# Performance work log

Measured on AMD Instinct MI355X. Metric: run time of the kernel, lower is better.

The kernel has to match this reference:

```python
import jax, jax.numpy as jnp
import numpy as np

NUM_EXPERTS = 8
TOP_K = 2
N_TOKENS = 4096
HIDDEN = 1024
EXPERT_DIM = 4096


def setup_inputs() -> dict:
    key = jax.random.key(0)
    ks = jax.random.split(key, 4)
    x = jax.random.normal(ks[0], (N_TOKENS, HIDDEN), dtype=jnp.float32)
    Wg = jax.random.normal(ks[1], (HIDDEN, NUM_EXPERTS), dtype=jnp.float32) * 0.02
    bg = jnp.zeros((NUM_EXPERTS,), dtype=jnp.float32)
    W1 = jax.random.normal(ks[2], (NUM_EXPERTS, HIDDEN, EXPERT_DIM), dtype=jnp.float32) * 0.02
    b1 = jnp.zeros((NUM_EXPERTS, EXPERT_DIM), dtype=jnp.float32)
    W2 = jax.random.normal(ks[3], (NUM_EXPERTS, EXPERT_DIM, HIDDEN), dtype=jnp.float32) * 0.02
    b2 = jnp.zeros((NUM_EXPERTS, HIDDEN), dtype=jnp.float32)
    return {"x": x, "Wg": Wg, "bg": bg, "W1": W1, "b1": b1, "W2": W2, "b2": b2}


def reference(x, Wg, bg, W1, b1, W2, b2):
    # Gating: softmax over experts, then top-k routing with renormalized gates.
    gate_probs = jax.nn.softmax(x @ Wg + bg, axis=-1)          # [N, E]
    top_gates, top_idx = jax.lax.top_k(gate_probs, TOP_K)      # [N, K]
    top_gates = top_gates / jnp.sum(top_gates, axis=-1, keepdims=True)
    # Per-(token, expert) combine weight: sum of gates routed to that expert.
    combine = jnp.sum(
        jax.nn.one_hot(top_idx, NUM_EXPERTS, dtype=x.dtype) * top_gates[..., None],
        axis=1,
    )  # [N, E]
    # Expert MLPs: Linear -> ReLU -> Linear (dropout=0 at eval, norm=False).
    out = jnp.zeros_like(x)
    for e in range(NUM_EXPERTS):
        h = jax.nn.relu(x @ W1[e] + b1[e])                      # [N, expert_dim]
        y = h @ W2[e] + b2[e]                                   # [N, hidden]
        out = out + combine[:, e:e + 1] * y
    # Switch-style auxiliary load-balancing loss.
    expert_counts = jnp.sum(gate_probs, axis=0)                 # [E]
    expert_fractions = expert_counts / jnp.sum(expert_counts)
    gate_means = jnp.mean(gate_probs, axis=0)
    aux_loss = NUM_EXPERTS * jnp.sum(expert_fractions * gate_means)
    return out, aux_loss
```

## Files before the change

kernel.cpp:

```cpp
#include <hip/hip_runtime.h>


typedef unsigned short u16;
typedef __bf16 bf16x8 __attribute__((ext_vector_type(8)));
typedef float  f32x4  __attribute__((ext_vector_type(4)));

#define NTOK 4096
#define HID  1024
#define EDIM 4096
#define NEXP 8
#define MAXMT 72

__device__ __forceinline__ u16 f32_bf16(float f) {
  unsigned int u = __float_as_uint(f);
  u += 0x7FFFu + ((u >> 16) & 1u);
  return (u16)(u >> 16);
}

__global__ void gate_kernel(const float* __restrict__ x,
                            const float* __restrict__ Wg,
                            const float* __restrict__ bg,
                            float* __restrict__ combine,
                            float* __restrict__ counts,
                            int* __restrict__ icnt,
                            int* __restrict__ top2idx,
                            float* __restrict__ top2g,
                            u16* __restrict__ xbf) {
  __shared__ float lc[NEXP];
  int t = threadIdx.x;
  if (t < NEXP) lc[t] = 0.f;
  __syncthreads();
  int token = blockIdx.x * 4 + (t >> 6);
  int lane = t & 63;
  float s[NEXP] = {};
  const float* xr = x + (size_t)token * HID;
  u16* xb = xbf + (size_t)token * HID;
  for (int h = lane; h < HID; h += 64) {
    float xv = xr[h];
    xb[h] = f32_bf16(xv);
    const float* wrow = Wg + (size_t)h * NEXP;
#pragma unroll
    for (int e = 0; e < NEXP; ++e) s[e] += xv * wrow[e];
  }
#pragma unroll
  for (int off = 32; off > 0; off >>= 1) {
#pragma unroll
    for (int e = 0; e < NEXP; ++e) s[e] += __shfl_xor(s[e], off);
  }
  float m = -1e30f;
#pragma unroll
  for (int e = 0; e < NEXP; ++e) { s[e] += bg[e]; m = fmaxf(m, s[e]); }
  float p[NEXP]; float sum = 0.f;
#pragma unroll
  for (int e = 0; e < NEXP; ++e) { p[e] = expf(s[e] - m); sum += p[e]; }
  float inv = 1.f / sum;
#pragma unroll
  for (int e = 0; e < NEXP; ++e) p[e] *= inv;
  int i1 = 0; float g1 = p[0];
#pragma unroll
  for (int e = 1; e < NEXP; ++e) if (p[e] > g1) { g1 = p[e]; i1 = e; }
  int i2 = -1; float g2 = -1.f;
#pragma unroll
  for (int e = 0; e < NEXP; ++e) if (e != i1 && p[e] > g2) { g2 = p[e]; i2 = e; }
  float ginv = 1.f / (g1 + g2);
  if (lane == 0) {
#pragma unroll
    for (int e = 0; e < NEXP; ++e) {
      float c = (e == i1) ? g1 * ginv : (e == i2) ? g2 * ginv : 0.f;
      combine[(size_t)token * NEXP + e] = c;
      atomicAdd(&lc[e], p[e]);
    }
    top2idx[token * 2] = i1; top2idx[token * 2 + 1] = i2;
    top2g[token * 2] = g1 * ginv; top2g[token * 2 + 1] = g2 * ginv;
    atomicAdd(&icnt[i1], 1); atomicAdd(&icnt[i2], 1);
  }
  __syncthreads();
  if (t < NEXP) atomicAdd(&counts[t], lc[t]);
}

__global__ void aux_kernel(const float* __restrict__ counts, float* __restrict__ aux_out) {
  float s = 0.f;
#pragma unroll
  for (int e = 0; e < NEXP; ++e) s += counts[e];
  float a = 0.f;
#pragma unroll
  for (int e = 0; e < NEXP; ++e) a += (counts[e] / s) * (counts[e] / (float)NTOK);
  aux_out[0] = (float)NEXP * a;
}

__global__ void route_kernel(const int* __restrict__ icnt,
                             const float* __restrict__ counts,
                             const int* __restrict__ top2idx,
                             int* __restrict__ nmtP,
                             int* __restrict__ mtE, int* __restrict__ mtRow0,
                             int* __restrict__ mtValid,
                             int* __restrict__ tok,
                             float* __restrict__ aux_out) {
  __shared__ int l_off[NEXP];
  __shared__ int l_cur[NEXP];
  int t = threadIdx.x;
  if (t == 0) {
    int s = 0, nm = 0;
    for (int e = 0; e < NEXP; ++e) {
      l_off[e] = s; l_cur[e] = 0;
      int c = icnt[e];
      int tiles = (c + 127) >> 7;
      for (int mt = 0; mt < tiles; ++mt) {
        mtE[nm] = e; mtRow0[nm] = s + (mt << 7);
        int v = c - (mt << 7); mtValid[nm] = v > 128 ? 128 : v;
        nm++;
      }
      s += c;
    }
    nmtP[0] = nm;
    float fs = 0.f;
    for (int e = 0; e < NEXP; ++e) fs += counts[e];
    float a = 0.f;
    for (int e = 0; e < NEXP; ++e) a += (counts[e] / fs) * (counts[e] / (float)NTOK);
    aux_out[0] = (float)NEXP * a;
  }
  __syncthreads();
  for (int i = t; i < NTOK * 2; i += 256) {
    int e = top2idx[i];
    int pos = atomicAdd(&l_cur[e], 1);
    tok[l_off[e] + pos] = (i >> 1) | ((i & 1) << 16);
  }
}

__global__ __launch_bounds__(256) void cvtT_kernel(const float* __restrict__ W,
                                                   u16* __restrict__ WT, int R, int C) {
  __shared__ u16 tile[64][66];
  int t = threadIdx.x;
  size_t eoff = (size_t)blockIdx.z * R * C;
  int c0 = blockIdx.x * 64, r0 = blockIdx.y * 64;
  const float* Wp = W + eoff + (size_t)r0 * C + c0;
  u16* WTp = WT + eoff + (size_t)c0 * R + r0;
#pragma unroll
  for (int p = 0; p < 4; ++p) {
    int idx = p * 256 + t;
    int row = idx >> 4;
    int col = (idx & 15) * 4;
    float4 v = *(const float4*)(Wp + (size_t)row * C + col);
    tile[row][col + 0] = f32_bf16(v.x);
    tile[row][col + 1] = f32_bf16(v.y);
    tile[row][col + 2] = f32_bf16(v.z);
    tile[row][col + 3] = f32_bf16(v.w);
  }
  __syncthreads();
#pragma unroll
  for (int p = 0; p < 4; ++p) {
    int idx = p * 256 + t;
    int oc = idx >> 4;
    int orow = (idx & 15) * 4;
    ushort4 o;
    o.x = tile[orow + 0][oc];
    o.y = tile[orow + 1][oc];
    o.z = tile[orow + 2][oc];
    o.w = tile[orow + 3][oc];
    *(ushort4*)(WTp + (size_t)oc * R + orow) = o;
  }
}

template<int MODE, int SPLITK>
__global__ __launch_bounds__(256) void gemm_sparse(
    const u16* __restrict__ A, const u16* __restrict__ Wt,
    const int* __restrict__ nmtP, const int* __restrict__ mtE,
    const int* __restrict__ mtRow0, const int* __restrict__ mtValid,
    const int* __restrict__ tok,
    const float* __restrict__ bias, u16* __restrict__ Hout,
    float* __restrict__ Y0, float* __restrict__ Y1)
{
  constexpr int KDIM = (MODE == 1) ? HID : EDIM;
  constexpr int NDIM = (MODE == 1) ? EDIM : HID;
  constexpr int NT = NDIM / 128;
  constexpr int NK = KDIM / 32 / SPLITK;

  const int nwg = gridDim.x;
  const int q = nwg >> 3, rr8 = nwg & 7;
  const int xcd = blockIdx.x & 7, jj = blockIdx.x >> 3;
  int item = (xcd < rr8 ? xcd * (q + 1) : rr8 * (q + 1) + (xcd - rr8) * q) + jj;

  if (item >= nmtP[0] * NT * SPLITK) return;
  const int gmt = item / (NT * SPLITK);
  const int sk  = (item / NT) % SPLITK;
  const int nt  = item % NT;
  const int e = mtE[gmt], row0 = mtRow0[gmt], valid = mtValid[gmt];
  const int kbeg = sk * (KDIM / SPLITK);

  __shared__ __align__(16) u16 As[3][128 * 32];
  __shared__ __align__(16) u16 Bs[3][128 * 32];
  const int t = threadIdx.x;
  const int lane = t & 63;
  const int w = t >> 6;
  const int wr = w >> 1, wc = w & 1;
  const int bn0 = nt << 7;
  const int kq = lane >> 4;
  const int r  = lane & 15;

  const u16* Bb = Wt + ((size_t)e * NDIM + bn0) * KDIM;

  size_t arow[2];
  int srow[2];
#pragma unroll
  for (int c = 0; c < 2; ++c) {
    int idx = c * 256 + t;
    int row = idx >> 2;
    srow[c] = row;
    if (MODE == 1) {
      int rw = (row < valid) ? row : 0;
      arow[c] = (size_t)(tok[row0 + rw] & 0xFFFF) * KDIM;
    } else {
      arow[c] = (size_t)(row0 + row) * KDIM;
    }
  }

  auto stage = [&](int buf, int k0) {
#pragma unroll
    for (int c = 0; c < 2; ++c) {
      int idx = c * 256 + t;
      int row = idx >> 2;
      int kc  = (((idx & 3) ^ ((row >> 1) & 3))) << 3;
      __builtin_amdgcn_global_load_lds(
          (const __attribute__((address_space(1))) void*)(A + arow[c] + k0 + kc),
          (__attribute__((address_space(3))) void*)(&As[buf][idx * 8]), 16, 0, 0);
      __builtin_amdgcn_global_load_lds(
          (const __attribute__((address_space(1))) void*)(Bb + (size_t)srow[c] * KDIM + k0 + kc),
          (__attribute__((address_space(3))) void*)(&Bs[buf][idx * 8]), 16, 0, 0);
    }
  };

  f32x4 acc[4][4] = {};

  stage(0, kbeg);
  stage(1, kbeg + 32);
  int cb = 0, sb = 2;
  for (int ks = 0; ks < NK; ++ks) {
    if (ks + 1 < NK) asm volatile("s_waitcnt vmcnt(4)" ::: "memory");
    else             asm volatile("s_waitcnt vmcnt(0)" ::: "memory");
    __builtin_amdgcn_s_barrier();
    __builtin_amdgcn_sched_barrier(0);
    if (ks + 2 < NK) stage(sb, kbeg + (ks + 2) * 32);

    bf16x8 af[4], bfr[4];
#pragma unroll
    for (int f = 0; f < 4; ++f) {
      int ra = wr * 64 + f * 16 + r;
      af[f]  = *(const bf16x8*)(&As[cb][ra * 32 + ((kq ^ ((ra >> 1) & 3)) << 3)]);
      int rb = wc * 64 + f * 16 + r;
      bfr[f] = *(const bf16x8*)(&Bs[cb][rb * 32 + ((kq ^ ((rb >> 1) & 3)) << 3)]);
    }
    __builtin_amdgcn_s_setprio(1);
#pragma unroll
    for (int fm = 0; fm < 4; ++fm) {
#pragma unroll
      for (int fn = 0; fn < 4; ++fn) {
        acc[fn][fm] = __builtin_amdgcn_mfma_f32_16x16x32_bf16(bfr[fn], af[fm], acc[fn][fm], 0, 0, 0);
      }
    }
    __builtin_amdgcn_s_setprio(0);
    cb = (cb == 2) ? 0 : cb + 1;
    sb = (sb == 2) ? 0 : sb + 1;
  }

  if (MODE == 1) {
#pragma unroll
    for (int fm = 0; fm < 4; ++fm) {
      int lr = wr * 64 + fm * 16 + r;
      if (lr < valid) {
        u16* hrow = Hout + (size_t)(row0 + lr) * EDIM;
#pragma unroll
        for (int fn = 0; fn < 4; ++fn) {
          int col0 = bn0 + wc * 64 + fn * 16 + kq * 4;
          float4 bv = *(const float4*)(bias + (size_t)e * EDIM + col0);
          float v0 = acc[fn][fm][0] + bv.x; v0 = v0 > 0.f ? v0 : 0.f;
          float v1 = acc[fn][fm][1] + bv.y; v1 = v1 > 0.f ? v1 : 0.f;
          float v2 = acc[fn][fm][2] + bv.z; v2 = v2 > 0.f ? v2 : 0.f;
          float v3 = acc[fn][fm][3] + bv.w; v3 = v3 > 0.f ? v3 : 0.f;
          ushort4 h = make_ushort4(f32_bf16(v0), f32_bf16(v1), f32_bf16(v2), f32_bf16(v3));
          *(ushort4*)(hrow + col0) = h;
        }
      }
    }
  } else {
    float* Yb = (sk == 0) ? Y0 : Y1;
#pragma unroll
    for (int fm = 0; fm < 4; ++fm) {
      int lr = wr * 64 + fm * 16 + r;
      if (lr < valid) {
        int entry = tok[row0 + lr];
        int tt = entry & 0xFFFF, ss = entry >> 16;
        float* yrow = Yb + ((size_t)ss * NTOK + tt) * HID;
#pragma unroll
        for (int fn = 0; fn < 4; ++fn) {
          int col0 = bn0 + wc * 64 + fn * 16 + kq * 4;
          float4 o;
          if (sk == 0) {
            float4 bv = *(const float4*)(bias + (size_t)e * HID + col0);
            o.x = acc[fn][fm][0] + bv.x;
            o.y = acc[fn][fm][1] + bv.y;
            o.z = acc[fn][fm][2] + bv.z;
            o.w = acc[fn][fm][3] + bv.w;
          } else {
            o.x = acc[fn][fm][0];
            o.y = acc[fn][fm][1];
            o.z = acc[fn][fm][2];
            o.w = acc[fn][fm][3];
          }
          *(float4*)(yrow + col0) = o;
        }
      }
    }
  }
}

__global__ void final_kernel(const float* __restrict__ top2g,
                             const float* __restrict__ Ys0,
                             const float* __restrict__ Ys1,
                             float* __restrict__ out) {
  size_t idx4 = (size_t)blockIdx.x * 256 + threadIdx.x;
  size_t base = idx4 * 4;
  int t = (int)(base >> 10);
  float g0 = top2g[t * 2], g1 = top2g[t * 2 + 1];
  float4 a0 = *(const float4*)(Ys0 + base);
  float4 b0 = *(const float4*)(Ys1 + base);
  float4 a1 = *(const float4*)(Ys0 + (size_t)NTOK * HID + base);
  float4 b1 = *(const float4*)(Ys1 + (size_t)NTOK * HID + base);
  float4 o;
  o.x = g0 * (a0.x + b0.x) + g1 * (a1.x + b1.x);
  o.y = g0 * (a0.y + b0.y) + g1 * (a1.y + b1.y);
  o.z = g0 * (a0.z + b0.z) + g1 * (a1.z + b1.z);
  o.w = g0 * (a0.w + b0.w) + g1 * (a1.w + b1.w);
  *(float4*)(out + base) = o;
}

__global__ void init_out_kernel(const float* __restrict__ combine,
                                const float* __restrict__ b2,
                                float* __restrict__ out) {
  size_t idx = (size_t)blockIdx.x * 256 + threadIdx.x;
  int i = (int)(idx >> 10), j = (int)(idx & 1023);
  float v = 0.f;
#pragma unroll
  for (int e = 0; e < NEXP; ++e) v += combine[(size_t)i * NEXP + e] * b2[e * HID + j];
  out[idx] = v;
}

template<int MODE>
__global__ __launch_bounds__(256) void gemm_kernel(
    const u16* __restrict__ A, const u16* __restrict__ BT,
    int M, int N, int K,
    const float* __restrict__ bias, u16* __restrict__ Hout,
    const float* __restrict__ combine, int expert, float* __restrict__ Out)
{
  __shared__ __align__(16) u16 As[128 * 32];
  __shared__ __align__(16) u16 Bs[128 * 32];
  const int t = threadIdx.x;
  const int lane = t & 63;
  const int w = t >> 6;
  const int wr = w >> 1, wc = w & 1;
  const int nbn = N >> 7;
  const int bm0 = (int)(blockIdx.x / nbn) << 7;
  const int bn0 = (int)(blockIdx.x % nbn) << 7;
  const int kq = lane >> 4;
  const int r  = lane & 15;
  f32x4 acc[4][4] = {};
  const u16* Ab = A + (size_t)bm0 * K;
  const u16* Bb = BT + (size_t)bn0 * K;
  for (int k0 = 0; k0 < K; k0 += 32) {
    __syncthreads();
#pragma unroll
    for (int c = 0; c < 2; ++c) {
      int idx = c * 256 + t;
      int row = idx >> 2;
      int kc  = (idx & 3) << 3;
      __builtin_amdgcn_global_load_lds(
          (const __attribute__((address_space(1))) void*)(Ab + (size_t)row * K + k0 + kc),
          (__attribute__((address_space(3))) void*)(As + idx * 8), 16, 0, 0);
      __builtin_amdgcn_global_load_lds(
          (const __attribute__((address_space(1))) void*)(Bb + (size_t)row * K + k0 + kc),
          (__attribute__((address_space(3))) void*)(Bs + idx * 8), 16, 0, 0);
    }
    __syncthreads();
    bf16x8 af[4], bfr[4];
#pragma unroll
    for (int f = 0; f < 4; ++f) {
      af[f]  = *(const bf16x8*)(As + (wr * 64 + f * 16 + r) * 32 + kq * 8);
      bfr[f] = *(const bf16x8*)(Bs + (wc * 64 + f * 16 + r) * 32 + kq * 8);
    }
#pragma unroll
    for (int fm = 0; fm < 4; ++fm) {
#pragma unroll
      for (int fn = 0; fn < 4; ++fn) {
        acc[fm][fn] = __builtin_amdgcn_mfma_f32_16x16x32_bf16(af[fm], bfr[fn], acc[fm][fn], 0, 0, 0);
      }
    }
  }
  if (MODE == 1) {
#pragma unroll
    for (int fn = 0; fn < 4; ++fn) {
      int col = bn0 + wc * 64 + fn * 16 + r;
      float bv = bias[col];
#pragma unroll
      for (int fm = 0; fm < 4; ++fm) {
#pragma unroll
        for (int j = 0; j < 4; ++j) {
          int row = bm0 + wr * 64 + fm * 16 + kq * 4 + j;
          float v = acc[fm][fn][j] + bv;
          v = v > 0.f ? v : 0.f;
          Hout[(size_t)row * N + col] = f32_bf16(v);
        }
      }
    }
  } else {
#pragma unroll
    for (int fm = 0; fm < 4; ++fm) {
      float cg[4];
#pragma unroll
      for (int j = 0; j < 4; ++j) {
        int row = bm0 + wr * 64 + fm * 16 + kq * 4 + j;
        cg[j] = combine[(size_t)row * NEXP + expert];
      }
#pragma unroll
      for (int fn = 0; fn < 4; ++fn) {
        int col = bn0 + wc * 64 + fn * 16 + r;
#pragma unroll
        for (int j = 0; j < 4; ++j) {
          int row = bm0 + wr * 64 + fm * 16 + kq * 4 + j;
          Out[(size_t)row * N + col] += cg[j] * acc[fm][fn][j];
        }
      }
    }
  }
}

extern "C" void kernel_launch(void* const* d_in, const int* in_sizes, int n_in,
                              void* d_out, int out_size, void* d_ws, size_t ws_size,
                              hipStream_t stream) {
  (void)in_sizes; (void)n_in; (void)out_size;
  const float* x  = (const float*)d_in[0];
  const float* Wg = (const float*)d_in[1];
  const float* bg = (const float*)d_in[2];
  const float* W1 = (const float*)d_in[3];
  const float* b1 = (const float*)d_in[4];
  const float* W2 = (const float*)d_in[5];
  const float* b2 = (const float*)d_in[6];
  float* out = (float*)d_out;

  char* ws = (char*)d_ws;
  float* counts  = (float*)(ws);
  int*   icnt    = (int*)(ws + 64);
  int*   nmtP    = (int*)(ws + 256);
  int*   mtE     = (int*)(ws + 512);
  int*   mtRow0  = (int*)(ws + 1024);
  int*   mtValid = (int*)(ws + 1536);
  int*   top2idx = (int*)(ws + 4096);
  float* top2g   = (float*)(ws + 36864);
  int*   tok     = (int*)(ws + 69632);
  float* combine = (float*)(ws + 131072);

  const size_t MB = 1024 * 1024;
  u16* xbf = (u16*)(ws + 1 * MB);

  const size_t REQ = 241 * MB;
  bool sparse = ws_size >= REQ;

  hipMemsetAsync(ws, 0, 1024, stream);
  gate_kernel<<<NTOK / 4, 256, 0, stream>>>(x, Wg, bg, combine, counts, icnt,
                                            top2idx, top2g, xbf);

  if (sparse) {
    u16* w1tA    = (u16*)(ws + 9 * MB);
    u16* w2tA    = (u16*)(ws + 73 * MB);
    u16* H       = (u16*)(ws + 137 * MB);
    float* Ys0   = (float*)(ws + 209 * MB);
    float* Ys1   = (float*)(ws + 9 * MB);

    cvtT_kernel<<<dim3(EDIM / 64, HID / 64, NEXP), 256, 0, stream>>>(W1, w1tA, HID, EDIM);
    cvtT_kernel<<<dim3(HID / 64, EDIM / 64, NEXP), 256, 0, stream>>>(W2, w2tA, EDIM, HID);
    route_kernel<<<1, 256, 0, stream>>>(icnt, counts, top2idx, nmtP, mtE, mtRow0,
                                        mtValid, tok, out + (size_t)NTOK * HID);

    gemm_sparse<1, 1><<<MAXMT * (EDIM / 128), 256, 0, stream>>>(
        xbf, w1tA, nmtP, mtE, mtRow0, mtValid, tok, b1, H, nullptr, nullptr);
    gemm_sparse<2, 2><<<MAXMT * (HID / 128) * 2, 256, 0, stream>>>(
        H, w2tA, nmtP, mtE, mtRow0, mtValid, tok, b2, nullptr, Ys0, Ys1);
    final_kernel<<<(NTOK * HID / 4) / 256, 256, 0, stream>>>(top2g, Ys0, Ys1, out);
  } else {
    u16* w1t = (u16*)(ws + 9 * MB);
    u16* w2t = (u16*)(ws + 17 * MB);
    u16* H   = (u16*)(ws + 25 * MB);
    aux_kernel<<<1, 1, 0, stream>>>(counts, out + (size_t)NTOK * HID);
    init_out_kernel<<<(NTOK * HID) / 256, 256, 0, stream>>>(combine, b2, out);
    for (int e = 0; e < NEXP; ++e) {
      cvtT_kernel<<<dim3(EDIM / 64, HID / 64, 1), 256, 0, stream>>>(
          W1 + (size_t)e * HID * EDIM, w1t, HID, EDIM);
      gemm_kernel<1><<<(NTOK / 128) * (EDIM / 128), 256, 0, stream>>>(
          xbf, w1t, NTOK, EDIM, HID, b1 + (size_t)e * EDIM, H, nullptr, 0, nullptr);
      cvtT_kernel<<<dim3(HID / 64, EDIM / 64, 1), 256, 0, stream>>>(
          W2 + (size_t)e * EDIM * HID, w2t, EDIM, HID);
      gemm_kernel<2><<<(NTOK / 128) * (HID / 128), 256, 0, stream>>>(
          H, w2t, NTOK, HID, EDIM, nullptr, nullptr, combine, e, out);
    }
  }
}
```

Baseline: 465.7 us.

## Use 256x256 tiled 512-thread kernel for first expert GEMM

Adds a dedicated first-layer GEMM kernel using 256x256 output tiles with 512 threads, BK=64, double-buffered direct global-to-LDS loads with XOR swizzle. The route kernel now also builds a 256-row tile list per expert. The larger tile raises arithmetic intensity and reduces redundant loads of weights and gathered activations. In exchange it uses 128KB of LDS and occupancy of one block, and the coarser tiles waste more padded rows per expert.

```diff
diff --git a/kernel.cpp b/kernel.cpp
--- a/kernel.cpp
+++ b/kernel.cpp
@@ -10,6 +10,7 @@
 #define EDIM 4096
 #define NEXP 8
 #define MAXMT 72
+#define MAXMT2 40
 
 __device__ __forceinline__ u16 f32_bf16(float f) {
   unsigned int u = __float_as_uint(f);
@@ -94,13 +95,16 @@
                              int* __restrict__ nmtP,
                              int* __restrict__ mtE, int* __restrict__ mtRow0,
                              int* __restrict__ mtValid,
+                             int* __restrict__ nmtP2,
+                             int* __restrict__ mtE2, int* __restrict__ mtRow02,
+                             int* __restrict__ mtValid2,
                              int* __restrict__ tok,
                              float* __restrict__ aux_out) {
   __shared__ int l_off[NEXP];
   __shared__ int l_cur[NEXP];
   int t = threadIdx.x;
   if (t == 0) {
-    int s = 0, nm = 0;
+    int s = 0, nm = 0, nm2 = 0;
     for (int e = 0; e < NEXP; ++e) {
       l_off[e] = s; l_cur[e] = 0;
       int c = icnt[e];
@@ -110,9 +114,16 @@
         int v = c - (mt << 7); mtValid[nm] = v > 128 ? 128 : v;
         nm++;
       }
+      int tiles2 = (c + 255) >> 8;
+      for (int mt = 0; mt < tiles2; ++mt) {
+        mtE2[nm2] = e; mtRow02[nm2] = s + (mt << 8);
+        int v = c - (mt << 8); mtValid2[nm2] = v > 256 ? 256 : v;
+        nm2++;
+      }
       s += c;
     }
     nmtP[0] = nm;
+    nmtP2[0] = nm2;
     float fs = 0.f;
     for (int e = 0; e < NEXP; ++e) fs += counts[e];
     float a = 0.f;
@@ -158,6 +169,129 @@
     o.z = tile[orow + 2][oc];
     o.w = tile[orow + 3][oc];
     *(ushort4*)(WTp + (size_t)oc * R + orow) = o;
+  }
+}
+
+__global__ __launch_bounds__(512, 1) void gemm1_256(
+    const u16* __restrict__ A, const u16* __restrict__ Wt,
+    const int* __restrict__ nmtP2, const int* __restrict__ mtE2,
+    const int* __restrict__ mtRow02, const int* __restrict__ mtValid2,
+    const int* __restrict__ tok,
+    const float* __restrict__ bias, u16* __restrict__ Hout)
+{
+  constexpr int KDIM = HID;
+  constexpr int NT   = EDIM / 256;
+  constexpr int NKT  = KDIM / 64;
+
+  const int nwg = gridDim.x;
+  const int q = nwg >> 3, rr8 = nwg & 7;
+  const int xcd = blockIdx.x & 7, jj = blockIdx.x >> 3;
+  int item = (xcd < rr8 ? xcd * (q + 1) : rr8 * (q + 1) + (xcd - rr8) * q) + jj;
+
+  if (item >= nmtP2[0] * NT) return;
+  const int gmt = item / NT;
+  const int nt  = item % NT;
+  const int e = mtE2[gmt], row0 = mtRow02[gmt], valid = mtValid2[gmt];
+  const int bn0 = nt << 8;
+
+  __shared__ __align__(16) u16 As[2][256 * 64];
+  __shared__ __align__(16) u16 Bs[2][256 * 64];
+
+  const int t = threadIdx.x;
+  const int lane = t & 63;
+  const int w = t >> 6;
+  const int wr = w >> 2, wc = w & 3;
+  const int kq = lane >> 4;
+  const int r  = lane & 15;
+  const int srow = t >> 3;
+  const int schunk = t & 7;
+
+  const u16* Bb = Wt + ((size_t)e * EDIM + bn0) * KDIM;
+
+  size_t arow[4];
+#pragma unroll
+  for (int c = 0; c < 4; ++c) {
+    int row = c * 64 + srow;
+    int rw = (row < valid) ? row : 0;
+    arow[c] = (size_t)(tok[row0 + rw] & 0xFFFF) * KDIM;
+  }
+
+  auto stage = [&](int buf, int kt) {
+#pragma unroll
+    for (int c = 0; c < 4; ++c) {
+      int row = c * 64 + srow;
+      int kc = (schunk ^ (row & 7)) << 3;
+      __builtin_amdgcn_global_load_lds(
+          (const __attribute__((address_space(1))) void*)(A + arow[c] + kt * 64 + kc),
+          (__attribute__((address_space(3))) void*)(&As[buf][row * 64 + schunk * 8]), 16, 0, 0);
+    }
+#pragma unroll
+    for (int c = 0; c < 4; ++c) {
+      int row = c * 64 + srow;
+      int kc = (schunk ^ (row & 7)) << 3;
+      __builtin_amdgcn_global_load_lds(
+          (const __attribute__((address_space(1))) void*)(Bb + (size_t)row * KDIM + kt * 64 + kc),
+          (__attribute__((address_space(3))) void*)(&Bs[buf][row * 64 + schunk * 8]), 16, 0, 0);
+    }
+  };
+
+  f32x4 acc[4][8] = {};
+
+  stage(0, 0);
+  asm volatile("s_waitcnt vmcnt(0)" ::: "memory");
+  __builtin_amdgcn_s_barrier();
+
+  int cur = 0;
+  for (int kt = 0; kt < NKT; ++kt) {
+    const bool more = (kt + 1 < NKT);
+    if (more) stage(cur ^ 1, kt + 1);
+#pragma unroll
+    for (int kh = 0; kh < 2; ++kh) {
+      bf16x8 af[8], bfr[4];
+      const int ck = kh * 4 + kq;
+#pragma unroll
+      for (int f = 0; f < 8; ++f) {
+        int ra = wr * 128 + f * 16 + r;
+        af[f] = *(const bf16x8*)(&As[cur][ra * 64 + ((ck ^ (ra & 7)) << 3)]);
+      }
+#pragma unroll
+      for (int f = 0; f < 4; ++f) {
+        int rb = wc * 64 + f * 16 + r;
+        bfr[f] = *(const bf16x8*)(&Bs[cur][rb * 64 + ((ck ^ (rb & 7)) << 3)]);
+      }
+#pragma unroll
+      for (int fm = 0; fm < 8; ++fm) {
+#pragma unroll
+        for (int fn = 0; fn < 4; ++fn) {
+          acc[fn][fm] = __builtin_amdgcn_mfma_f32_16x16x32_bf16(bfr[fn], af[fm], acc[fn][fm], 0, 0, 0);
+        }
+      }
+    }
+    if (more) {
+      asm volatile("s_waitcnt lgkmcnt(0)" ::: "memory");
+      asm volatile("s_waitcnt vmcnt(0)" ::: "memory");
+      __builtin_amdgcn_s_barrier();
+      cur ^= 1;
+    }
+  }
+
+#pragma unroll
+  for (int fm = 0; fm < 8; ++fm) {
+    int lr = wr * 128 + fm * 16 + r;
+    if (lr < valid) {
+      u16* hrow = Hout + (size_t)(row0 + lr) * EDIM;
+#pragma unroll
+      for (int fn = 0; fn < 4; ++fn) {
+        int col0 = bn0 + wc * 64 + fn * 16 + kq * 4;
+        float4 bv = *(const float4*)(bias + (size_t)e * EDIM + col0);
+        float v0 = acc[fn][fm][0] + bv.x; v0 = v0 > 0.f ? v0 : 0.f;
+        float v1 = acc[fn][fm][1] + bv.y; v1 = v1 > 0.f ? v1 : 0.f;
+        float v2 = acc[fn][fm][2] + bv.z; v2 = v2 > 0.f ? v2 : 0.f;
+        float v3 = acc[fn][fm][3] + bv.w; v3 = v3 > 0.f ? v3 : 0.f;
+        ushort4 h = make_ushort4(f32_bf16(v0), f32_bf16(v1), f32_bf16(v2), f32_bf16(v3));
+        *(ushort4*)(hrow + col0) = h;
+      }
+    }
   }
 }
 
@@ -446,16 +580,20 @@
   float* out = (float*)d_out;
 
   char* ws = (char*)d_ws;
-  float* counts  = (float*)(ws);
-  int*   icnt    = (int*)(ws + 64);
-  int*   nmtP    = (int*)(ws + 256);
-  int*   mtE     = (int*)(ws + 512);
-  int*   mtRow0  = (int*)(ws + 1024);
-  int*   mtValid = (int*)(ws + 1536);
-  int*   top2idx = (int*)(ws + 4096);
-  float* top2g   = (float*)(ws + 36864);
-  int*   tok     = (int*)(ws + 69632);
-  float* combine = (float*)(ws + 131072);
+  float* counts   = (float*)(ws);
+  int*   icnt     = (int*)(ws + 64);
+  int*   nmtP     = (int*)(ws + 256);
+  int*   nmtP2    = (int*)(ws + 384);
+  int*   mtE      = (int*)(ws + 512);
+  int*   mtRow0   = (int*)(ws + 1024);
+  int*   mtValid  = (int*)(ws + 1536);
+  int*   mtE2     = (int*)(ws + 2048);
+  int*   mtRow02  = (int*)(ws + 2304);
+  int*   mtValid2 = (int*)(ws + 2560);
+  int*   top2idx  = (int*)(ws + 4096);
+  float* top2g    = (float*)(ws + 36864);
+  int*   tok      = (int*)(ws + 69632);
+  float* combine  = (float*)(ws + 131072);
 
   const size_t MB = 1024 * 1024;
   u16* xbf = (u16*)(ws + 1 * MB);
@@ -477,10 +615,11 @@
     cvtT_kernel<<<dim3(EDIM / 64, HID / 64, NEXP), 256, 0, stream>>>(W1, w1tA, HID, EDIM);
     cvtT_kernel<<<dim3(HID / 64, EDIM / 64, NEXP), 256, 0, stream>>>(W2, w2tA, EDIM, HID);
     route_kernel<<<1, 256, 0, stream>>>(icnt, counts, top2idx, nmtP, mtE, mtRow0,
-                                        mtValid, tok, out + (size_t)NTOK * HID);
-
-    gemm_sparse<1, 1><<<MAXMT * (EDIM / 128), 256, 0, stream>>>(
-        xbf, w1tA, nmtP, mtE, mtRow0, mtValid, tok, b1, H, nullptr, nullptr);
+                                        mtValid, nmtP2, mtE2, mtRow02, mtValid2,
+                                        tok, out + (size_t)NTOK * HID);
+
+    gemm1_256<<<MAXMT2 * (EDIM / 256), 512, 0, stream>>>(
+        xbf, w1tA, nmtP2, mtE2, mtRow02, mtValid2, tok, b1, H);
     gemm_sparse<2, 2><<<MAXMT * (HID / 128) * 2, 256, 0, stream>>>(
         H, w2tA, nmtP, mtE, mtRow0, mtValid, tok, b2, nullptr, Ys0, Ys1);
     final_kernel<<<(NTOK * HID / 4) / 256, 256, 0, stream>>>(top2g, Ys0, Ys1, out);
```

New measurement: 491.6 us. 1.06x slower.
